# Kernel tuning notes

Measured on AMD Instinct MI355X. Metric: run time of the kernel, lower is better.

## Reference

```python
import jax, jax.numpy as jnp
import numpy as np
import math

B, S, D, H = 4, 2048, 1024, 16
DH = D // H  # 64


def setup_inputs() -> dict:
    key = jax.random.key(0)
    ks = jax.random.split(key, 7)
    scale = 1.0 / math.sqrt(D)
    q = jax.random.normal(ks[0], (B, S, D), dtype=jnp.float32)
    k = jax.random.normal(ks[1], (B, S, D), dtype=jnp.float32)
    v = jax.random.normal(ks[2], (B, S, D), dtype=jnp.float32)
    mask = jnp.tril(jnp.ones((S, S), dtype=jnp.int32))[None, None]  # [1,1,S,S] causal
    wq = jax.random.normal(ks[3], (D, D), dtype=jnp.float32) * scale
    wk = jax.random.normal(ks[4], (D, D), dtype=jnp.float32) * scale
    wv = jax.random.normal(ks[5], (D, D), dtype=jnp.float32) * scale
    wo = jax.random.normal(ks[6], (D, D), dtype=jnp.float32) * scale
    return {"q": q, "k": k, "v": v, "mask": mask, "wq": wq, "wk": wk, "wv": wv, "wo": wo}


def reference(q, k, v, mask, wq, wk, wv, wo):
    # nn.Linear(bias=False): y = x @ W.T
    qry = q @ wq.T
    key = k @ wk.T
    val = v @ wv.T
    # [B,S,D] -> [B,H,S,DH]
    qry = qry.reshape(B, S, H, DH).transpose(0, 2, 1, 3)
    key = key.reshape(B, S, H, DH).transpose(0, 2, 1, 3)
    val = val.reshape(B, S, H, DH).transpose(0, 2, 1, 3)
    scores = jnp.einsum('bhqd,bhkd->bhqk', qry, key) / math.sqrt(DH)
    scores = jnp.where(mask == 0, jnp.float32(-1e9), scores)
    attn = jax.nn.softmax(scores, axis=-1)  # dropout p=0.0 -> identity
    x = jnp.einsum('bhqk,bhkd->bhqd', attn, val)
    x = x.transpose(0, 2, 1, 3).reshape(B, S, D)
    return x @ wo.T
```

## Files before the change

kernel.cpp:

```cpp
#include <hip/hip_runtime.h>
#include <hip/hip_bf16.h>

typedef __attribute__((ext_vector_type(8))) short bf16x8;
typedef __attribute__((ext_vector_type(4))) float f32x4;
typedef __attribute__((ext_vector_type(16))) float f32x16;

#define MFMA16(a, b, c) __builtin_amdgcn_mfma_f32_16x16x32_bf16((a), (b), (c), 0, 0, 0)
#define MFMA32(a, b, c) __builtin_amdgcn_mfma_f32_32x32x16_bf16((a), (b), (c), 0, 0, 0)

#if defined(__has_builtin)
#if __has_builtin(__builtin_amdgcn_exp2f)
#define EXP2(x) __builtin_amdgcn_exp2f(x)
#endif
#endif
#ifndef EXP2
#define EXP2(x) exp2f(x)
#endif

__device__ __forceinline__ short f2b(float f) {
  unsigned u = __builtin_bit_cast(unsigned, f);
  u += 0x7FFFu + ((u >> 16) & 1u);
  return (short)(u >> 16);
}
__device__ __forceinline__ unsigned cvtpk(float lo, float hi) {
  unsigned r;
  asm("v_cvt_pk_bf16_f32 %0, %1, %2" : "=v"(r) : "v"(lo), "v"(hi));
  return r;
}

__global__ __launch_bounds__(256) void cvt3_bf16(const float* __restrict__ s0,
                                                 const float* __restrict__ s1,
                                                 const float* __restrict__ s2,
                                                 short* __restrict__ d, long stride) {
  const int which = blockIdx.y;
  const float* s = which == 0 ? s0 : (which == 1 ? s1 : s2);
  long i = (long)blockIdx.x * 256 + threadIdx.x;
  const float4* sp = (const float4*)s;
  float4 a = sp[2 * i], b = sp[2 * i + 1];
  bf16x8 o;
  o[0] = f2b(a.x); o[1] = f2b(a.y); o[2] = f2b(a.z); o[3] = f2b(a.w);
  o[4] = f2b(b.x); o[5] = f2b(b.y); o[6] = f2b(b.z); o[7] = f2b(b.w);
  *(bf16x8*)(d + which * stride + i * 8) = o;
}
__global__ __launch_bounds__(256) void cvt4_bf16(const float* __restrict__ s0,
                                                 const float* __restrict__ s1,
                                                 const float* __restrict__ s2,
                                                 const float* __restrict__ s3,
                                                 short* __restrict__ d, long stride) {
  const int which = blockIdx.y;
  const float* s = which == 0 ? s0 : (which == 1 ? s1 : (which == 2 ? s2 : s3));
  long i = (long)blockIdx.x * 256 + threadIdx.x;
  const float4* sp = (const float4*)s;
  float4 a = sp[2 * i], b = sp[2 * i + 1];
  bf16x8 o;
  o[0] = f2b(a.x); o[1] = f2b(a.y); o[2] = f2b(a.z); o[3] = f2b(a.w);
  o[4] = f2b(b.x); o[5] = f2b(b.y); o[6] = f2b(b.z); o[7] = f2b(b.w);
  *(bf16x8*)(d + which * stride + i * 8) = o;
}

template <int MODE>
__global__ __launch_bounds__(256) void gemm_bt(const short* __restrict__ A_,
                                               const short* __restrict__ BT_,
                                               void* __restrict__ Cout,
                                               float oscale) {
  __shared__ __align__(16) short As[2][128 * 64];
  __shared__ __align__(16) short Bs[2][128 * 64];
  const int t = threadIdx.x;
  const int l = t & 63, w = t >> 6;
  const int grp = l >> 4, li = l & 15;
  const int wg = (((int)blockIdx.x & 7) << 6) | ((int)blockIdx.x >> 3);
  const int bm = wg >> 3, bn = wg & 7;
  const int m0 = bm << 7, n0 = bn << 7;
  const int wm = (w >> 1) << 6, wn = (w & 1) << 6;
  const int srow = t >> 3, scol = (t & 7) << 3;
  f32x4 acc[4][4] = {};
#pragma unroll
  for (int i = 0; i < 4; ++i) {
    const short* ga = A_ + (long)(m0 + i * 32 + srow) * 1024 + scol;
    __builtin_amdgcn_global_load_lds(
        (const __attribute__((address_space(1))) void*)ga,
        (__attribute__((address_space(3))) void*)&As[0][i * 2048 + t * 8], 16, 0, 0);
    const short* gb = BT_ + (long)(n0 + i * 32 + srow) * 1024 + scol;
    __builtin_amdgcn_global_load_lds(
        (const __attribute__((address_space(1))) void*)gb,
        (__attribute__((address_space(3))) void*)&Bs[0][i * 2048 + t * 8], 16, 0, 0);
  }
  __syncthreads();
#pragma unroll 1
  for (int kt = 0; kt < 16; ++kt) {
    const int cur = kt & 1;
    if (kt + 1 < 16) {
#pragma unroll
      for (int i = 0; i < 4; ++i) {
        const short* ga = A_ + (long)(m0 + i * 32 + srow) * 1024 + (kt + 1) * 64 + scol;
        __builtin_amdgcn_global_load_lds(
            (const __attribute__((address_space(1))) void*)ga,
            (__attribute__((address_space(3))) void*)&As[cur ^ 1][i * 2048 + t * 8], 16, 0, 0);
        const short* gb = BT_ + (long)(n0 + i * 32 + srow) * 1024 + (kt + 1) * 64 + scol;
        __builtin_amdgcn_global_load_lds(
            (const __attribute__((address_space(1))) void*)gb,
            (__attribute__((address_space(3))) void*)&Bs[cur ^ 1][i * 2048 + t * 8], 16, 0, 0);
      }
    }
#pragma unroll
    for (int kk = 0; kk < 64; kk += 32) {
      bf16x8 af[4], bfr[4];
#pragma unroll
      for (int mi = 0; mi < 4; ++mi)
        af[mi] = *(const bf16x8*)&As[cur][(wm + mi * 16 + li) * 64 + kk + grp * 8];
#pragma unroll
      for (int ni = 0; ni < 4; ++ni)
        bfr[ni] = *(const bf16x8*)&Bs[cur][(wn + ni * 16 + li) * 64 + kk + grp * 8];
#pragma unroll
      for (int mi = 0; mi < 4; ++mi)
#pragma unroll
        for (int ni = 0; ni < 4; ++ni)
          acc[mi][ni] = MFMA16(af[mi], bfr[ni], acc[mi][ni]);
    }
    __syncthreads();
  }
#pragma unroll
  for (int mi = 0; mi < 4; ++mi) {
#pragma unroll
    for (int ni = 0; ni < 4; ++ni) {
      f32x4 v = acc[mi][ni];
      int n = n0 + wn + ni * 16 + li;
#pragma unroll
      for (int r = 0; r < 4; ++r) {
        int m = m0 + wm + mi * 16 + grp * 4 + r;
        if (MODE == 2) {
          ((float*)Cout)[(long)m * 1024 + n] = v[r];
        } else {
          int b = m >> 11, sq = m & 2047;
          int h = n >> 6, dh = n & 63;
          if (MODE == 0)
            ((short*)Cout)[(((long)(b * 16 + h) * 2048 + sq) << 6) + dh] = f2b(v[r] * oscale);
          else
            ((short*)Cout)[(((long)(b * 16 + h) * 64 + dh) << 11) + sq] = f2b(v[r]);
        }
      }
    }
  }
}

__device__ __forceinline__ void attn_tile(const short* Kbuf, const short* Vbuf,
                                          const bf16x8 qf[4], f32x16& oa, f32x16& ob,
                                          float& mrun, float& lsum, int kt, bool diag,
                                          int khmax, int qg, int q, int hi) {
  f32x16 p0 = {}, p1 = {};
  __builtin_amdgcn_s_setprio(1);
#pragma unroll
  for (int kd = 0; kd < 4; ++kd) {
    int colB = kd * 32 + hi * 16;
    bf16x8 kf0 = *(const bf16x8*)((const char*)Kbuf + q * 128 + (colB ^ ((q & 7) << 4)));
    p0 = MFMA32(kf0, qf[kd], p0);
  }
  if (khmax == 2) {
#pragma unroll
    for (int kd = 0; kd < 4; ++kd) {
      int colB = kd * 32 + hi * 16;
      bf16x8 kf1 = *(const bf16x8*)((const char*)Kbuf + (q + 32) * 128 + (colB ^ ((q & 7) << 4)));
      p1 = MFMA32(kf1, qf[kd], p1);
    }
  }
  __builtin_amdgcn_s_setprio(0);
  if (diag) {
#pragma unroll
    for (int r = 0; r < 16; ++r) {
      int key0 = kt * 64 + (r & 3) + 8 * (r >> 2) + 4 * hi;
      if (key0 > qg) p0[r] = -1e30f;
      if (key0 + 32 > qg) p1[r] = -1e30f;
    }
  }
  float pm = p0[0];
#pragma unroll
  for (int r = 1; r < 16; ++r) pm = fmaxf(pm, p0[r]);
  if (khmax == 2) {
#pragma unroll
    for (int r = 0; r < 16; ++r) pm = fmaxf(pm, p1[r]);
  }
  pm = fmaxf(pm, __shfl_xor(pm, 32));
  const bool skip = __all(pm - mrun <= 11.5f);
  float mn;
  float alpha = 1.f;
  if (skip) {
    mn = mrun;
  } else {
    mn = fmaxf(mrun, pm);
    alpha = EXP2(mrun - mn);
    mrun = mn;
  }
  float ts = 0.f;
#pragma unroll
  for (int r = 0; r < 16; ++r) { p0[r] = EXP2(p0[r] - mn); ts += p0[r]; }
  if (khmax == 2) {
#pragma unroll
    for (int r = 0; r < 16; ++r) { p1[r] = EXP2(p1[r] - mn); ts += p1[r]; }
  }
  ts += __shfl_xor(ts, 32);
  if (skip) {
    lsum += ts;
  } else {
    lsum = lsum * alpha + ts;
#pragma unroll
    for (int r = 0; r < 16; ++r) { oa[r] *= alpha; ob[r] *= alpha; }
  }
  unsigned own0[8], prt0[8], own1[8], prt1[8];
#pragma unroll
  for (int g = 0; g < 4; ++g) {
    own0[2 * g]     = cvtpk(p0[4 * g], p0[4 * g + 1]);
    own0[2 * g + 1] = cvtpk(p0[4 * g + 2], p0[4 * g + 3]);
  }
#pragma unroll
  for (int i = 0; i < 8; ++i) prt0[i] = __shfl_xor(own0[i], 32);
  if (khmax == 2) {
#pragma unroll
    for (int g = 0; g < 4; ++g) {
      own1[2 * g]     = cvtpk(p1[4 * g], p1[4 * g + 1]);
      own1[2 * g + 1] = cvtpk(p1[4 * g + 2], p1[4 * g + 3]);
    }
#pragma unroll
    for (int i = 0; i < 8; ++i) prt1[i] = __shfl_xor(own1[i], 32);
  }
  __builtin_amdgcn_s_setprio(1);
#define PVSTEP(KD, OWN, PRT)                                                              \
  {                                                                                       \
    const int kdl = (KD) & 1;                                                             \
    unsigned b0 = hi ? PRT[4 * kdl + 2] : OWN[4 * kdl];                                   \
    unsigned b1 = hi ? PRT[4 * kdl + 3] : OWN[4 * kdl + 1];                               \
    unsigned b2 = hi ? OWN[4 * kdl + 2] : PRT[4 * kdl];                                   \
    unsigned b3 = hi ? OWN[4 * kdl + 3] : PRT[4 * kdl + 1];                               \
    int4 bi = {(int)b0, (int)b1, (int)b2, (int)b3};                                       \
    bf16x8 pb = __builtin_bit_cast(bf16x8, bi);                                           \
    int colB = (KD) * 32 + hi * 16;                                                       \
    bf16x8 vf0 = *(const bf16x8*)((const char*)Vbuf + q * 128 + (colB ^ ((q & 7) << 4))); \
    bf16x8 vf1 = *(const bf16x8*)((const char*)Vbuf + (q + 32) * 128 + (colB ^ ((q & 7) << 4))); \
    oa = MFMA32(vf0, pb, oa);                                                             \
    ob = MFMA32(vf1, pb, ob);                                                             \
  }
  PVSTEP(0, own0, prt0);
  PVSTEP(1, own0, prt0);
  if (khmax == 2) {
    PVSTEP(2, own1, prt1);
    PVSTEP(3, own1, prt1);
  }
#undef PVSTEP
  __builtin_amdgcn_s_setprio(0);
}

__global__ __launch_bounds__(256, 2) void attn_fwd(const short* __restrict__ Qh,
                                                   const short* __restrict__ Kh,
                                                   const short* __restrict__ Vt,
                                                   short* __restrict__ Xb) {
  __shared__ __align__(16) short Ks[2][4096];
  __shared__ __align__(16) short Vs[2][4096];
  const int bh = blockIdx.x;
  const int qtA = blockIdx.y;
  const int qtB = 15 - qtA;
  const int t = threadIdx.x, l = t & 63, w = t >> 6;
  const int q = l & 31, hi = l >> 5;
  const int q0wA = qtA * 128 + w * 32, q0wB = qtB * 128 + w * 32;
  const int qgA = q0wA + q, qgB = q0wB + q;
  const short* Qp = Qh + (long)bh * 131072;
  const char* Kb = (const char*)(Kh + (long)bh * 131072);
  const char* Vb = (const char*)(Vt + (long)bh * 131072);

  bf16x8 qfA[4], qfB[4];
#pragma unroll
  for (int kd = 0; kd < 4; ++kd) {
    qfA[kd] = *(const bf16x8*)(Qp + (long)qgA * 64 + kd * 16 + hi * 8);
    qfB[kd] = *(const bf16x8*)(Qp + (long)qgB * 64 + kd * 16 + hi * 8);
  }

  const int co0 = t * 16, co1 = co0 + 4096;

  f32x16 oaA = {}, obA = {}, oaB = {}, obB = {};
  float mrunA = -1e30f, lsumA = 0.f, mrunB = -1e30f, lsumB = 0.f;
  const int tripsA = (q0wA >> 6) + 1;
  const int tripsB = (q0wB >> 6) + 1;
  const int nt = 2 * qtB + 2;

#define STAGE(KT, BUF)                                                                   \
  {                                                                                      \
    long ktb = (long)(KT) * 8192;                                                        \
    _Pragma("unroll") for (int c = 0; c < 2; ++c) {                                      \
      int o = c ? co1 : co0;                                                             \
      int ksrc = o ^ (((o >> 7) & 7) << 4);                                              \
      __builtin_amdgcn_global_load_lds(                                                  \
          (const __attribute__((address_space(1))) void*)(Kb + ktb + ksrc),              \
          (__attribute__((address_space(3))) void*)((char*)Ks[BUF] + o), 16, 0, 0);      \
      int row = o >> 7, c16 = (o >> 4) & 7;                                              \
      int vsrc = row * 4096 + (KT) * 128 + (((c16 ^ (row & 7))) << 4);                   \
      __builtin_amdgcn_global_load_lds(                                                  \
          (const __attribute__((address_space(1))) void*)(Vb + vsrc),                    \
          (__attribute__((address_space(3))) void*)((char*)Vs[BUF] + o), 16, 0, 0);      \
    }                                                                                    \
  }

  STAGE(0, 0);
  __syncthreads();

  for (int kt = 0; kt < nt; ++kt) {
    const int buf = kt & 1;
    if (kt + 1 < nt) STAGE(kt + 1, buf ^ 1);

    if (kt < tripsB) {
      const bool diag = (kt == tripsB - 1);
      const int khmax = (diag && ((q0wB & 32) == 0)) ? 1 : 2;
      attn_tile(Ks[buf], Vs[buf], qfB, oaB, obB, mrunB, lsumB, kt, diag, khmax, qgB, q, hi);
    }
    if (kt < tripsA) {
      const bool diag = (kt == tripsA - 1);
      const int khmax = (diag && ((q0wA & 32) == 0)) ? 1 : 2;
      attn_tile(Ks[buf], Vs[buf], qfA, oaA, obA, mrunA, lsumA, kt, diag, khmax, qgA, q, hi);
    }
    __syncthreads();
  }

  const int b = bh >> 4, h = bh & 15;
#define EPI(OA, OB, LS, QG)                                                \
  {                                                                        \
    const float inv = 1.f / (LS);                                          \
    short* orow = Xb + (long)(b * 2048 + (QG)) * 1024 + h * 64;            \
    _Pragma("unroll") for (int g = 0; g < 4; ++g) {                        \
      unsigned u0 = cvtpk((OA)[4 * g] * inv, (OA)[4 * g + 1] * inv);       \
      unsigned u1 = cvtpk((OA)[4 * g + 2] * inv, (OA)[4 * g + 3] * inv);   \
      uint2 uu = {u0, u1};                                                 \
      *(uint2*)(orow + 8 * g + 4 * hi) = uu;                               \
      unsigned w0 = cvtpk((OB)[4 * g] * inv, (OB)[4 * g + 1] * inv);       \
      unsigned w1 = cvtpk((OB)[4 * g + 2] * inv, (OB)[4 * g + 3] * inv);   \
      uint2 ww = {w0, w1};                                                 \
      *(uint2*)(orow + 32 + 8 * g + 4 * hi) = ww;                          \
    }                                                                      \
  }
  EPI(oaA, obA, lsumA, qgA);
  EPI(oaB, obB, lsumB, qgB);
#undef EPI
}

extern "C" void kernel_launch(void* const* d_in, const int* in_sizes, int n_in,
                              void* d_out, int out_size, void* d_ws, size_t ws_size,
                              hipStream_t stream) {
  const float* q  = (const float*)d_in[0];
  const float* k  = (const float*)d_in[1];
  const float* v  = (const float*)d_in[2];
  const float* wq = (const float*)d_in[4];
  const float* wk = (const float*)d_in[5];
  const float* wv = (const float*)d_in[6];
  const float* wo = (const float*)d_in[7];

  short* ws = (short*)d_ws;
  const long T = 8388608;
  short* qb  = ws;
  short* kb  = qb + T;
  short* vb  = kb + T;
  short* Qh  = vb + T;
  short* Kh  = Qh + T;
  short* Vt  = Kh + T;
  short* Xb  = Vt + T;
  short* wqb = Xb + T;
  short* wkb = wqb + 1048576;
  short* wvb = wkb + 1048576;
  short* wob = wvb + 1048576;

  cvt3_bf16<<<dim3(4096, 3), 256, 0, stream>>>(q, k, v, qb, T);
  cvt4_bf16<<<dim3(512, 4), 256, 0, stream>>>(wq, wk, wv, wo, wqb, 1048576);

  gemm_bt<0><<<512, 256, 0, stream>>>(qb, wqb, (void*)Qh, 0.18033688f);
  gemm_bt<0><<<512, 256, 0, stream>>>(kb, wkb, (void*)Kh, 1.0f);
  gemm_bt<1><<<512, 256, 0, stream>>>(vb, wvb, (void*)Vt, 1.0f);
  attn_fwd<<<dim3(64, 8), 256, 0, stream>>>(Qh, Kh, Vt, Xb);
  gemm_bt<2><<<512, 256, 0, stream>>>(Xb, wob, (float*)d_out, 1.0f);
}
```

Before: 205.9 us.

## Split attention into smaller 128-thread blocks with single-buffered K/V tiles

Reworks the attention kernel so each 128-thread block handles one pair of 32-row query strips, one light and one heavy, over a 64×32 grid instead of 64×8 blocks of 256 threads. K/V staging drops from double-buffered to single-buffered LDS, with a barrier after every load. The intent is finer-grained load balancing and lower LDS use per block. In exchange, the two waves in each block compute the same rows twice because the wave index is no longer used, and the loads no longer overlap with compute.

Measured after the change: 295.6 us. 43.5% more time.

```diff
diff --git a/kernel.cpp b/kernel.cpp
--- a/kernel.cpp
+++ b/kernel.cpp
@@ -248,19 +248,18 @@
   __builtin_amdgcn_s_setprio(0);
 }
 
-__global__ __launch_bounds__(256, 2) void attn_fwd(const short* __restrict__ Qh,
+__global__ __launch_bounds__(128, 2) void attn_fwd(const short* __restrict__ Qh,
                                                    const short* __restrict__ Kh,
                                                    const short* __restrict__ Vt,
                                                    short* __restrict__ Xb) {
-  __shared__ __align__(16) short Ks[2][4096];
-  __shared__ __align__(16) short Vs[2][4096];
+  __shared__ __align__(16) short Ks[4096];
+  __shared__ __align__(16) short Vs[4096];
   const int bh = blockIdx.x;
-  const int qtA = blockIdx.y;
-  const int qtB = 15 - qtA;
-  const int t = threadIdx.x, l = t & 63, w = t >> 6;
+  const int a  = blockIdx.y;
+  const int t = threadIdx.x, l = t & 63;
   const int q = l & 31, hi = l >> 5;
-  const int q0wA = qtA * 128 + w * 32, q0wB = qtB * 128 + w * 32;
-  const int qgA = q0wA + q, qgB = q0wB + q;
+  const int sA = a, sB = 63 - a;
+  const int qgA = sA * 32 + q, qgB = sB * 32 + q;
   const short* Qp = Qh + (long)bh * 131072;
   const char* Kb = (const char*)(Kh + (long)bh * 131072);
   const char* Vb = (const char*)(Vt + (long)bh * 131072);
@@ -272,47 +271,37 @@
     qfB[kd] = *(const bf16x8*)(Qp + (long)qgB * 64 + kd * 16 + hi * 8);
   }
 
-  const int co0 = t * 16, co1 = co0 + 4096;
-
   f32x16 oaA = {}, obA = {}, oaB = {}, obB = {};
   float mrunA = -1e30f, lsumA = 0.f, mrunB = -1e30f, lsumB = 0.f;
-  const int tripsA = (q0wA >> 6) + 1;
-  const int tripsB = (q0wB >> 6) + 1;
-  const int nt = 2 * qtB + 2;
-
-#define STAGE(KT, BUF)                                                                   \
-  {                                                                                      \
-    long ktb = (long)(KT) * 8192;                                                        \
-    _Pragma("unroll") for (int c = 0; c < 2; ++c) {                                      \
-      int o = c ? co1 : co0;                                                             \
-      int ksrc = o ^ (((o >> 7) & 7) << 4);                                              \
-      __builtin_amdgcn_global_load_lds(                                                  \
-          (const __attribute__((address_space(1))) void*)(Kb + ktb + ksrc),              \
-          (__attribute__((address_space(3))) void*)((char*)Ks[BUF] + o), 16, 0, 0);      \
-      int row = o >> 7, c16 = (o >> 4) & 7;                                              \
-      int vsrc = row * 4096 + (KT) * 128 + (((c16 ^ (row & 7))) << 4);                   \
-      __builtin_amdgcn_global_load_lds(                                                  \
-          (const __attribute__((address_space(1))) void*)(Vb + vsrc),                    \
-          (__attribute__((address_space(3))) void*)((char*)Vs[BUF] + o), 16, 0, 0);      \
-    }                                                                                    \
-  }
-
-  STAGE(0, 0);
-  __syncthreads();
+  const int tripsA = (sA >> 1) + 1;
+  const int tripsB = (sB >> 1) + 1;
+  const int nt = tripsB;
 
   for (int kt = 0; kt < nt; ++kt) {
-    const int buf = kt & 1;
-    if (kt + 1 < nt) STAGE(kt + 1, buf ^ 1);
-
-    if (kt < tripsB) {
+#pragma unroll
+    for (int c = 0; c < 4; ++c) {
+      int o = t * 16 + c * 2048;
+      int ksrc = o ^ (((o >> 7) & 7) << 4);
+      __builtin_amdgcn_global_load_lds(
+          (const __attribute__((address_space(1))) void*)(Kb + (long)kt * 8192 + ksrc),
+          (__attribute__((address_space(3))) void*)((char*)Ks + o), 16, 0, 0);
+      int row = o >> 7, c16 = (o >> 4) & 7;
+      int vsrc = row * 4096 + kt * 128 + ((c16 ^ (row & 7)) << 4);
+      __builtin_amdgcn_global_load_lds(
+          (const __attribute__((address_space(1))) void*)(Vb + vsrc),
+          (__attribute__((address_space(3))) void*)((char*)Vs + o), 16, 0, 0);
+    }
+    __syncthreads();
+
+    {
       const bool diag = (kt == tripsB - 1);
-      const int khmax = (diag && ((q0wB & 32) == 0)) ? 1 : 2;
-      attn_tile(Ks[buf], Vs[buf], qfB, oaB, obB, mrunB, lsumB, kt, diag, khmax, qgB, q, hi);
+      const int khmax = (diag && !(sB & 1)) ? 1 : 2;
+      attn_tile(Ks, Vs, qfB, oaB, obB, mrunB, lsumB, kt, diag, khmax, qgB, q, hi);
     }
     if (kt < tripsA) {
       const bool diag = (kt == tripsA - 1);
-      const int khmax = (diag && ((q0wA & 32) == 0)) ? 1 : 2;
-      attn_tile(Ks[buf], Vs[buf], qfA, oaA, obA, mrunA, lsumA, kt, diag, khmax, qgA, q, hi);
+      const int khmax = (diag && !(sA & 1)) ? 1 : 2;
+      attn_tile(Ks, Vs, qfA, oaA, obA, mrunA, lsumA, kt, diag, khmax, qgA, q, hi);
     }
     __syncthreads();
   }
@@ -369,6 +358,6 @@
   gemm_bt<0><<<512, 256, 0, stream>>>(qb, wqb, (void*)Qh, 0.18033688f);
   gemm_bt<0><<<512, 256, 0, stream>>>(kb, wkb, (void*)Kh, 1.0f);
   gemm_bt<1><<<512, 256, 0, stream>>>(vb, wvb, (void*)Vt, 1.0f);
-  attn_fwd<<<dim3(64, 8), 256, 0, stream>>>(Qh, Kh, Vt, Xb);
+  attn_fwd<<<dim3(64, 32), 128, 0, stream>>>(Qh, Kh, Vt, Xb);
   gemm_bt<2><<<512, 256, 0, stream>>>(Xb, wob, (float*)d_out, 1.0f);
 }
```

## Fuse fp32-to-bf16 activation conversion into projection GEMM loads

Applied to the files above, without the earlier changes.

Removes the separate cvt3_bf16 pass over q/k/v. The projection GEMMs now read fp32 activations directly, prefetch the next k-tile into registers, and convert and store them to LDS after the MFMA loop. This avoids writing and rereading 48MB of bf16 intermediates. The cost is twice the global read bytes per A tile, higher register pressure, and register-staged loads in place of direct global-to-LDS loads for A.

Result: faster. 201.1 us (-2.4%).

```diff
diff --git a/kernel.cpp b/kernel.cpp
--- a/kernel.cpp
+++ b/kernel.cpp
@@ -27,21 +27,13 @@
   asm("v_cvt_pk_bf16_f32 %0, %1, %2" : "=v"(r) : "v"(lo), "v"(hi));
   return r;
 }
-
-__global__ __launch_bounds__(256) void cvt3_bf16(const float* __restrict__ s0,
-                                                 const float* __restrict__ s1,
-                                                 const float* __restrict__ s2,
-                                                 short* __restrict__ d, long stride) {
-  const int which = blockIdx.y;
-  const float* s = which == 0 ? s0 : (which == 1 ? s1 : s2);
-  long i = (long)blockIdx.x * 256 + threadIdx.x;
-  const float4* sp = (const float4*)s;
-  float4 a = sp[2 * i], b = sp[2 * i + 1];
+__device__ __forceinline__ bf16x8 cvt8(float4 a, float4 b) {
   bf16x8 o;
   o[0] = f2b(a.x); o[1] = f2b(a.y); o[2] = f2b(a.z); o[3] = f2b(a.w);
   o[4] = f2b(b.x); o[5] = f2b(b.y); o[6] = f2b(b.z); o[7] = f2b(b.w);
-  *(bf16x8*)(d + which * stride + i * 8) = o;
-}
+  return o;
+}
+
 __global__ __launch_bounds__(256) void cvt4_bf16(const float* __restrict__ s0,
                                                  const float* __restrict__ s1,
                                                  const float* __restrict__ s2,
@@ -51,18 +43,14 @@
   const float* s = which == 0 ? s0 : (which == 1 ? s1 : (which == 2 ? s2 : s3));
   long i = (long)blockIdx.x * 256 + threadIdx.x;
   const float4* sp = (const float4*)s;
-  float4 a = sp[2 * i], b = sp[2 * i + 1];
-  bf16x8 o;
-  o[0] = f2b(a.x); o[1] = f2b(a.y); o[2] = f2b(a.z); o[3] = f2b(a.w);
-  o[4] = f2b(b.x); o[5] = f2b(b.y); o[6] = f2b(b.z); o[7] = f2b(b.w);
-  *(bf16x8*)(d + which * stride + i * 8) = o;
+  *(bf16x8*)(d + which * stride + i * 8) = cvt8(sp[2 * i], sp[2 * i + 1]);
 }
 
 template <int MODE>
-__global__ __launch_bounds__(256) void gemm_bt(const short* __restrict__ A_,
-                                               const short* __restrict__ BT_,
-                                               void* __restrict__ Cout,
-                                               float oscale) {
+__global__ __launch_bounds__(256) void gemm_proj(const float* __restrict__ A_,
+                                                 const short* __restrict__ BT_,
+                                                 short* __restrict__ Cout,
+                                                 float oscale) {
   __shared__ __align__(16) short As[2][128 * 64];
   __shared__ __align__(16) short Bs[2][128 * 64];
   const int t = threadIdx.x;
@@ -74,6 +62,92 @@
   const int wm = (w >> 1) << 6, wn = (w & 1) << 6;
   const int srow = t >> 3, scol = (t & 7) << 3;
   f32x4 acc[4][4] = {};
+
+  {
+#pragma unroll
+    for (int i = 0; i < 4; ++i) {
+      const float* ga = A_ + (long)(m0 + i * 32 + srow) * 1024 + scol;
+      float4 a0 = *(const float4*)ga, a1 = *(const float4*)(ga + 4);
+      *(bf16x8*)&As[0][i * 2048 + t * 8] = cvt8(a0, a1);
+      const short* gb = BT_ + (long)(n0 + i * 32 + srow) * 1024 + scol;
+      __builtin_amdgcn_global_load_lds(
+          (const __attribute__((address_space(1))) void*)gb,
+          (__attribute__((address_space(3))) void*)&Bs[0][i * 2048 + t * 8], 16, 0, 0);
+    }
+  }
+  __syncthreads();
+#pragma unroll 1
+  for (int kt = 0; kt < 16; ++kt) {
+    const int cur = kt & 1;
+    float4 pf[4][2];
+    if (kt + 1 < 16) {
+#pragma unroll
+      for (int i = 0; i < 4; ++i) {
+        const float* ga = A_ + (long)(m0 + i * 32 + srow) * 1024 + (kt + 1) * 64 + scol;
+        pf[i][0] = *(const float4*)ga;
+        pf[i][1] = *(const float4*)(ga + 4);
+        const short* gb = BT_ + (long)(n0 + i * 32 + srow) * 1024 + (kt + 1) * 64 + scol;
+        __builtin_amdgcn_global_load_lds(
+            (const __attribute__((address_space(1))) void*)gb,
+            (__attribute__((address_space(3))) void*)&Bs[cur ^ 1][i * 2048 + t * 8], 16, 0, 0);
+      }
+    }
+#pragma unroll
+    for (int kk = 0; kk < 64; kk += 32) {
+      bf16x8 af[4], bfr[4];
+#pragma unroll
+      for (int mi = 0; mi < 4; ++mi)
+        af[mi] = *(const bf16x8*)&As[cur][(wm + mi * 16 + li) * 64 + kk + grp * 8];
+#pragma unroll
+      for (int ni = 0; ni < 4; ++ni)
+        bfr[ni] = *(const bf16x8*)&Bs[cur][(wn + ni * 16 + li) * 64 + kk + grp * 8];
+#pragma unroll
+      for (int mi = 0; mi < 4; ++mi)
+#pragma unroll
+        for (int ni = 0; ni < 4; ++ni)
+          acc[mi][ni] = MFMA16(af[mi], bfr[ni], acc[mi][ni]);
+    }
+    if (kt + 1 < 16) {
+#pragma unroll
+      for (int i = 0; i < 4; ++i)
+        *(bf16x8*)&As[cur ^ 1][i * 2048 + t * 8] = cvt8(pf[i][0], pf[i][1]);
+    }
+    __syncthreads();
+  }
+#pragma unroll
+  for (int mi = 0; mi < 4; ++mi) {
+#pragma unroll
+    for (int ni = 0; ni < 4; ++ni) {
+      f32x4 v = acc[mi][ni];
+      int n = n0 + wn + ni * 16 + li;
+#pragma unroll
+      for (int r = 0; r < 4; ++r) {
+        int m = m0 + wm + mi * 16 + grp * 4 + r;
+        int b = m >> 11, sq = m & 2047;
+        int h = n >> 6, dh = n & 63;
+        if (MODE == 0)
+          Cout[(((long)(b * 16 + h) * 2048 + sq) << 6) + dh] = f2b(v[r] * oscale);
+        else
+          Cout[(((long)(b * 16 + h) * 64 + dh) << 11) + sq] = f2b(v[r]);
+      }
+    }
+  }
+}
+
+__global__ __launch_bounds__(256) void gemm_out(const short* __restrict__ A_,
+                                                const short* __restrict__ BT_,
+                                                float* __restrict__ Cout) {
+  __shared__ __align__(16) short As[2][128 * 64];
+  __shared__ __align__(16) short Bs[2][128 * 64];
+  const int t = threadIdx.x;
+  const int l = t & 63, w = t >> 6;
+  const int grp = l >> 4, li = l & 15;
+  const int wg = (((int)blockIdx.x & 7) << 6) | ((int)blockIdx.x >> 3);
+  const int bm = wg >> 3, bn = wg & 7;
+  const int m0 = bm << 7, n0 = bn << 7;
+  const int wm = (w >> 1) << 6, wn = (w & 1) << 6;
+  const int srow = t >> 3, scol = (t & 7) << 3;
+  f32x4 acc[4][4] = {};
 #pragma unroll
   for (int i = 0; i < 4; ++i) {
     const short* ga = A_ + (long)(m0 + i * 32 + srow) * 1024 + scol;
@@ -128,16 +202,7 @@
 #pragma unroll
       for (int r = 0; r < 4; ++r) {
         int m = m0 + wm + mi * 16 + grp * 4 + r;
-        if (MODE == 2) {
-          ((float*)Cout)[(long)m * 1024 + n] = v[r];
-        } else {
-          int b = m >> 11, sq = m & 2047;
-          int h = n >> 6, dh = n & 63;
-          if (MODE == 0)
-            ((short*)Cout)[(((long)(b * 16 + h) * 2048 + sq) << 6) + dh] = f2b(v[r] * oscale);
-          else
-            ((short*)Cout)[(((long)(b * 16 + h) * 64 + dh) << 11) + sq] = f2b(v[r]);
-        }
+        Cout[(long)m * 1024 + n] = v[r];
       }
     }
   }
@@ -351,10 +416,7 @@
 
   short* ws = (short*)d_ws;
   const long T = 8388608;
-  short* qb  = ws;
-  short* kb  = qb + T;
-  short* vb  = kb + T;
-  short* Qh  = vb + T;
+  short* Qh  = ws;
   short* Kh  = Qh + T;
   short* Vt  = Kh + T;
   short* Xb  = Vt + T;
@@ -363,12 +425,11 @@
   short* wvb = wkb + 1048576;
   short* wob = wvb + 1048576;
 
-  cvt3_bf16<<<dim3(4096, 3), 256, 0, stream>>>(q, k, v, qb, T);
   cvt4_bf16<<<dim3(512, 4), 256, 0, stream>>>(wq, wk, wv, wo, wqb, 1048576);
 
-  gemm_bt<0><<<512, 256, 0, stream>>>(qb, wqb, (void*)Qh, 0.18033688f);
-  gemm_bt<0><<<512, 256, 0, stream>>>(kb, wkb, (void*)Kh, 1.0f);
-  gemm_bt<1><<<512, 256, 0, stream>>>(vb, wvb, (void*)Vt, 1.0f);
+  gemm_proj<0><<<512, 256, 0, stream>>>(q, wqb, Qh, 0.18033688f);
+  gemm_proj<0><<<512, 256, 0, stream>>>(k, wkb, Kh, 1.0f);
+  gemm_proj<1><<<512, 256, 0, stream>>>(v, wvb, Vt, 1.0f);
   attn_fwd<<<dim3(64, 8), 256, 0, stream>>>(Qh, Kh, Vt, Xb);
-  gemm_bt<2><<<512, 256, 0, stream>>>(Xb, wob, (float*)d_out, 1.0f);
-}
+  gemm_out<<<512, 256, 0, stream>>>(Xb, wob, (float*)d_out);
+}
```
